# Optimization experiments

Measured on AMD Instinct MI355X. Metric: run time of the kernel, lower is better.

## Reference

```python
import jax, jax.numpy as jnp
import numpy as np

FEATURE_W = 1.0
TRIPLET_W = 1.0
SOFT_W = 1.0
MARGIN = 0.2
TEMP = 1.0
COMMIT_W = 0.1
DISTORT_W = 0.1
STRIDE = 320

B, T, D, K = 8, 1500, 512, 4096


def setup_inputs() -> dict:
    key = jax.random.key(0)
    k1, k2, k3, k4, k5 = jax.random.split(key, 5)
    return {
        "student_features": jax.random.normal(k1, (B, T, D), dtype=jnp.float32),
        "teacher_features": jax.random.normal(k2, (B, T, D), dtype=jnp.float32),
        "teacher_codes": jax.random.randint(k3, (B, T), 0, K),
        "codebook": jax.random.normal(k4, (K, D), dtype=jnp.float32),
        "lengths": jax.random.randint(k5, (B,), 0, T * STRIDE),
    }


def _sq_dists(flat, codebook):
    x2 = jnp.sum(flat * flat, axis=-1, keepdims=True)          # (N,1)
    c2 = jnp.sum(codebook * codebook, axis=-1)[None, :]        # (1,K)
    xc = jnp.einsum("nd,kd->nk", flat, codebook)               # (N,K)
    return jnp.maximum(x2 + c2 - 2.0 * xc, 0.0)


def reference(student_features, teacher_features, teacher_codes, codebook, lengths):
    b, t, d = student_features.shape
    # valid-frame mask from sample lengths
    valid = jnp.minimum(lengths // STRIDE, t)                  # (B,)
    mask = (jnp.arange(t)[None, :] < valid[:, None]).astype(student_features.dtype)  # (B,T)
    msum = jnp.sum(mask)

    # feature loss: masked mean of per-token MSE
    diff = student_features - teacher_features
    feature_loss = jnp.sum(jnp.mean(diff * diff, axis=-1) * mask) / msum

    # triplet loss
    pos_dist = jnp.sqrt(jnp.sum(diff * diff, axis=-1))
    neg_teacher = jnp.roll(teacher_features, shift=1, axis=0)
    nd = student_features - neg_teacher
    neg_dist = jnp.sqrt(jnp.sum(nd * nd, axis=-1))
    triplet = jax.nn.relu(pos_dist - neg_dist + MARGIN)
    triplet_loss = jnp.sum(triplet * mask) / msum

    # soft token (KL distillation over codebook logits)
    s_flat = student_features.reshape(-1, d)                   # (B*T, D)
    t_flat = teacher_features.reshape(-1, d)
    s_logits = -_sq_dists(s_flat, codebook) / TEMP             # (B*T, K)
    t_logits = -_sq_dists(t_flat, codebook) / TEMP
    s_logp = jax.nn.log_softmax(s_logits, axis=-1)
    t_logp = jax.nn.log_softmax(t_logits, axis=-1)
    t_prob = jax.lax.stop_gradient(jnp.exp(t_logp))
    t_logp = jax.lax.stop_gradient(t_logp)
    kl_per_token = jnp.sum(t_prob * (t_logp - s_logp), axis=-1)  # (B*T,)
    flat_mask = mask.reshape(-1)
    soft_loss = jnp.sum(kl_per_token * flat_mask) / msum

    # VQ commitment / distortion (nearest-code quantization)
    codes = jnp.argmax(s_logits, axis=-1)                       # argmin dist == argmax logits
    quantized = codebook[codes].reshape(b, t, d)
    cdiff = student_features - jax.lax.stop_gradient(quantized)
    commitment_loss = jnp.mean(cdiff * cdiff)
    ddiff = jax.lax.stop_gradient(student_features) - quantized
    distortion_loss = jnp.mean(ddiff * ddiff)

    total = (FEATURE_W * feature_loss + TRIPLET_W * triplet_loss
             + SOFT_W * soft_loss + COMMIT_W * commitment_loss
             + DISTORT_W * distortion_loss)
    return total
```

## Files before the change

### kernel.cpp

```cpp
#include <hip/hip_runtime.h>

typedef unsigned short u16;
typedef unsigned int   u32;
typedef float  f32x16 __attribute__((ext_vector_type(16)));
typedef __bf16 bf16x8 __attribute__((ext_vector_type(8)));

#define B_N   8
#define T_N   1500
#define D_N   512
#define K_N   4096
#define NTOK  12000
#define STRD  320

#define X2S_OFF     0u
#define C2_OFF      49152u
#define FEATP_OFF   65536u
#define TRIPP_OFF   67584u
#define STATEP_OFF  71680u
#define SBF_OFF     557056u
#define TBF_OFF     (557056u + 12288000u)
#define CBBF_OFF    (557056u + 24576000u)


__device__ __forceinline__ u16 f2bf(float x){
  u32 u = __float_as_uint(x);
  u32 r = (u + 0x7fffu + ((u >> 16) & 1u)) >> 16;
  return (u16)r;
}

__device__ __forceinline__ void gl_lds16(const void* g, void* l){
  __builtin_amdgcn_global_load_lds(
      (__attribute__((address_space(1))) void*)(g),
      (__attribute__((address_space(3))) void*)(l),
      16, 0, 0);
}

__device__ __forceinline__ void merge_state(float& m, float& Z, float om, float oZ){
  float nm = fmaxf(m, om);
  Z = Z*__expf(m - nm) + oZ*__expf(om - nm);
  m = nm;
}
__device__ __forceinline__ void merge_stateT(float& m, float& Z, float& A,
                                             float om, float oZ, float oA){
  float nm = fmaxf(m, om);
  float e0 = __expf(m - nm), e1 = __expf(om - nm);
  Z = Z*e0 + oZ*e1; A = A*e0 + oA*e1; m = nm;
}

__global__ __launch_bounds__(256) void prep_kernel(
    const float* __restrict__ s, const float* __restrict__ t,
    const float* __restrict__ cb, const int* __restrict__ lengths,
    u16* __restrict__ sbf, u16* __restrict__ tbf, u16* __restrict__ cbbf,
    float* __restrict__ x2s, float* __restrict__ c2,
    float* __restrict__ featP, float* __restrict__ tripP)
{
  const int tid = threadIdx.x;
  const int w = tid >> 6, lane = tid & 63;
  __shared__ float sred[3][32];

  if (blockIdx.x < 375){
    const int tt = blockIdx.x;
    const int t8 = lane >> 3, kpart = lane & 7;
    const int tokL = w*8 + t8;
    const int n = tt*32 + tokL;
    const int b = n / T_N, tok = n - b*T_N;
    const int nr = ((b+7)&7)*T_N + tok;
    const float* srow = s + (size_t)n  * D_N;
    const float* trow = t + (size_t)n  * D_N;
    const float* rrow = t + (size_t)nr * D_N;

    float x2 = 0.f, sd2 = 0.f, nd2 = 0.f;
    uint4 sbq[8], tbq[8];
#pragma unroll
    for (int q = 0; q < 8; ++q){
      const int kl = q*64 + kpart*8;
      float4 a0 = *(const float4*)(srow + kl), a1 = *(const float4*)(srow + kl + 4);
      float4 b0 = *(const float4*)(trow + kl), b1 = *(const float4*)(trow + kl + 4);
      float4 r0 = *(const float4*)(rrow + kl), r1 = *(const float4*)(rrow + kl + 4);
      float sv[8] = {a0.x,a0.y,a0.z,a0.w,a1.x,a1.y,a1.z,a1.w};
      float tv[8] = {b0.x,b0.y,b0.z,b0.w,b1.x,b1.y,b1.z,b1.w};
      float rv[8] = {r0.x,r0.y,r0.z,r0.w,r1.x,r1.y,r1.z,r1.w};
      u16 sb[8], tb[8];
#pragma unroll
      for (int i = 0; i < 8; ++i){
        float d = sv[i] - tv[i]; sd2 += d*d;
        x2 += sv[i]*sv[i];
        float e = sv[i] - rv[i]; nd2 += e*e;
        sb[i] = f2bf(sv[i]); tb[i] = f2bf(tv[i]);
      }
      sbq[q].x = (u32)sb[0] | ((u32)sb[1]<<16); sbq[q].y = (u32)sb[2] | ((u32)sb[3]<<16);
      sbq[q].z = (u32)sb[4] | ((u32)sb[5]<<16); sbq[q].w = (u32)sb[6] | ((u32)sb[7]<<16);
      tbq[q].x = (u32)tb[0] | ((u32)tb[1]<<16); tbq[q].y = (u32)tb[2] | ((u32)tb[3]<<16);
      tbq[q].z = (u32)tb[4] | ((u32)tb[5]<<16); tbq[q].w = (u32)tb[6] | ((u32)tb[7]<<16);
    }
#pragma unroll
    for (int q = 0; q < 8; ++q){
      const int ks = q*4 + (kpart >> 1), kh = kpart & 1;
      const size_t chunk = ((size_t)tt*32 + ks)*64 + kh*32 + tokL;
      ((uint4*)sbf)[chunk] = sbq[q];
      ((uint4*)tbf)[chunk] = tbq[q];
    }
#pragma unroll
    for (int mm = 1; mm < 8; mm <<= 1){
      x2  += __shfl_xor(x2,  mm);
      sd2 += __shfl_xor(sd2, mm);
      nd2 += __shfl_xor(nd2, mm);
    }
    if (kpart == 0){ sred[0][tokL] = x2; sred[1][tokL] = sd2; sred[2][tokL] = nd2; }
    __syncthreads();
    if (tid < 32){
      float X2 = sred[0][tid], SD = sred[1][tid], ND = sred[2][tid];
      int n2 = tt*32 + tid, b2 = n2 / T_N, tk2 = n2 - b2*T_N;
      x2s[n2] = X2;
      int valid = lengths[b2] / STRD; if (valid > T_N) valid = T_N;
      float mf = (tk2 < valid) ? 1.f : 0.f;
      float fp = mf * SD * (1.f/512.f);
      float tp = mf * fmaxf(sqrtf(SD) - sqrtf(ND) + 0.2f, 0.f);
#pragma unroll
      for (int mm = 1; mm < 32; mm <<= 1){ fp += __shfl_xor(fp, mm); tp += __shfl_xor(tp, mm); }
      if (tid == 0){ featP[tt] = fp; tripP[tt] = tp; }
    }
  } else {
    const int idx = blockIdx.x - 375;
    const int ctile = idx*4 + w;
    const int kh = lane >> 5, sp = lane & 31;
    const int ch = ctile >> 6, cg = (ctile >> 3) & 7, ctg = ctile & 7;
    const int code = ctile*32 + sp;
    const float* crow = cb + (size_t)code * D_N;

    float s2 = 0.f;
#pragma unroll
    for (int stp = 0; stp < 32; ++stp){
      const int kc = stp >> 1, ks2 = stp & 1;
      const int k0 = stp*16 + kh*8;
      float4 c0 = *(const float4*)(crow + k0), c1 = *(const float4*)(crow + k0 + 4);
      float cv[8] = {c0.x,c0.y,c0.z,c0.w,c1.x,c1.y,c1.z,c1.w};
      u16 cbv[8];
#pragma unroll
      for (int i = 0; i < 8; ++i){ s2 += cv[i]*cv[i]; cbv[i] = f2bf(cv[i]); }
      uint4 pk;
      pk.x = (u32)cbv[0] | ((u32)cbv[1]<<16); pk.y = (u32)cbv[2] | ((u32)cbv[3]<<16);
      pk.z = (u32)cbv[4] | ((u32)cbv[5]<<16); pk.w = (u32)cbv[6] | ((u32)cbv[7]<<16);
      const size_t off = ((size_t)(ch*128 + cg*16 + kc))*8192 + ctg*1024 + ks2*512 + lane*8;
      *(uint4*)(cbbf + off) = pk;
    }
    s2 += __shfl_xor(s2, 32);
    if (lane < 32) c2[ctile*32 + lane] = s2;
  }
}

__global__ __launch_bounds__(256, 3) void main_kl_kernel(
    const u16* __restrict__ sbf, const u16* __restrict__ tbf,
    const u16* __restrict__ cbbf, const float* __restrict__ c2,
    float* __restrict__ stateP)
{
  __shared__ u16 Bb[2][8192];

  const int tid = threadIdx.x;
  const int w = tid >> 6, lane = tid & 63;
  const int kh = lane >> 5;
  const int tt = blockIdx.x >> 1, ch = blockIdx.x & 1;

  const u16* sA  = sbf  + (size_t)tt*16384;
  const u16* tA  = tbf  + (size_t)tt*16384;
  const u16* cbB = cbbf + (size_t)ch*1048576;

#pragma unroll
  for (int r = 0; r < 4; ++r){
    const int off = (r*256 + tid)*8;
    gl_lds16(cbB + off, &Bb[0][off]);
  }
  bf16x8 fS0 = *(const bf16x8*)(sA + lane*8);
  bf16x8 fS1 = *(const bf16x8*)(sA + 512 + lane*8);
  bf16x8 fT0 = *(const bf16x8*)(tA + lane*8);
  bf16x8 fT1 = *(const bf16x8*)(tA + 512 + lane*8);

  float mS = -3e38f, zS = 0.f, mT = -3e38f, zT = 0.f, aa = 0.f;
  f32x16 aS0, aS1, aT0, aT1;

  for (int c = 0; c < 128; ++c){
    const int kc = c & 15, p = c & 1;
    if (kc == 0){
#pragma unroll
      for (int i = 0; i < 16; ++i){ aS0[i]=0.f; aS1[i]=0.f; aT0[i]=0.f; aT1[i]=0.f; }
    }
    __syncthreads();
    if (c < 127){
      const u16* src = cbB + (size_t)(c+1)*8192;
#pragma unroll
      for (int r = 0; r < 4; ++r){
        const int off = (r*256 + tid)*8;
        gl_lds16(src + off, &Bb[p^1][off]);
      }
    }
    bf16x8 nS0 = fS0, nS1 = fS1, nT0 = fT0, nT1 = fT1;
    if (c < 127){
      const size_t kb = (size_t)((c+1) & 15) * 1024;
      nS0 = *(const bf16x8*)(sA + kb + lane*8);
      nS1 = *(const bf16x8*)(sA + kb + 512 + lane*8);
      nT0 = *(const bf16x8*)(tA + kb + lane*8);
      nT1 = *(const bf16x8*)(tA + kb + 512 + lane*8);
    }

    const u16* bp = &Bb[p][0];
    {
      bf16x8 c0 = *(const bf16x8*)(bp + (w*2+0)*1024 + lane*8);
      bf16x8 c1 = *(const bf16x8*)(bp + (w*2+0)*1024 + 512 + lane*8);
      aS0 = __builtin_amdgcn_mfma_f32_32x32x16_bf16(c0, fS0, aS0, 0, 0, 0);
      aT0 = __builtin_amdgcn_mfma_f32_32x32x16_bf16(c0, fT0, aT0, 0, 0, 0);
      aS0 = __builtin_amdgcn_mfma_f32_32x32x16_bf16(c1, fS1, aS0, 0, 0, 0);
      aT0 = __builtin_amdgcn_mfma_f32_32x32x16_bf16(c1, fT1, aT0, 0, 0, 0);
    }
    {
      bf16x8 c0 = *(const bf16x8*)(bp + (w*2+1)*1024 + lane*8);
      bf16x8 c1 = *(const bf16x8*)(bp + (w*2+1)*1024 + 512 + lane*8);
      aS1 = __builtin_amdgcn_mfma_f32_32x32x16_bf16(c0, fS0, aS1, 0, 0, 0);
      aT1 = __builtin_amdgcn_mfma_f32_32x32x16_bf16(c0, fT0, aT1, 0, 0, 0);
      aS1 = __builtin_amdgcn_mfma_f32_32x32x16_bf16(c1, fS1, aS1, 0, 0, 0);
      aT1 = __builtin_amdgcn_mfma_f32_32x32x16_bf16(c1, fT1, aT1, 0, 0, 0);
    }
    fS0 = nS0; fS1 = nS1; fT0 = nT0; fT1 = nT1;

    if (kc == 15){
      const int cg = c >> 4;
#pragma unroll
      for (int ct = 0; ct < 2; ++ct){
        const f32x16& vS = ct ? aS1 : aS0;
        const f32x16& vT = ct ? aT1 : aT0;
        const int ctg = w*2 + ct;
        const float* c2b = c2 + ch*2048 + cg*256 + ctg*32 + kh*4;
        float4 g0 = *(const float4*)(c2b);
        float4 g1 = *(const float4*)(c2b + 8);
        float4 g2 = *(const float4*)(c2b + 16);
        float4 g3 = *(const float4*)(c2b + 24);
        float c2v[16] = {g0.x,g0.y,g0.z,g0.w, g1.x,g1.y,g1.z,g1.w,
                         g2.x,g2.y,g2.z,g2.w, g3.x,g3.y,g3.z,g3.w};
        float sl[16], tl[16];
#pragma unroll
        for (int i = 0; i < 16; ++i){
          sl[i] = 2.0f*vS[i] - c2v[i];
          tl[i] = 2.0f*vT[i] - c2v[i];
        }
        float ms_t = sl[0], mt_t = tl[0];
#pragma unroll
        for (int i = 1; i < 16; ++i){ ms_t = fmaxf(ms_t, sl[i]); mt_t = fmaxf(mt_t, tl[i]); }
        float nmS = fmaxf(mS, ms_t), nmT = fmaxf(mT, mt_t);
        float esS = __expf(mS - nmS), esT = __expf(mT - nmT);
        zS *= esS; zT *= esT; aa *= esT;
#pragma unroll
        for (int i = 0; i < 16; ++i){
          zS += __expf(sl[i] - nmS);
          float e = __expf(tl[i] - nmT);
          zT += e; aa += e*(tl[i] - sl[i]);
        }
        mS = nmS; mT = nmT;
      }
    }
  }

  {
    float om = __shfl_xor(mS, 32), oZ = __shfl_xor(zS, 32);
    merge_state(mS, zS, om, oZ);
    float omt = __shfl_xor(mT, 32), ozt = __shfl_xor(zT, 32), oA = __shfl_xor(aa, 32);
    merge_stateT(mT, zT, aa, omt, ozt, oA);
  }
  __syncthreads();
  float* wst = (float*)&Bb[0][0];
  if (lane < 32){
    float* pw = wst + (w*32 + lane)*5;
    pw[0] = mS; pw[1] = zS; pw[2] = mT; pw[3] = zT; pw[4] = aa;
  }
  __syncthreads();
  if (tid < 32){
    const float* p0 = wst + tid*5;
    float m_s = p0[0], z_s = p0[1], m_t = p0[2], z_t = p0[3], a = p0[4];
#pragma unroll
    for (int ww = 1; ww < 4; ++ww){
      const float* pw = wst + (ww*32 + tid)*5;
      merge_state(m_s, z_s, pw[0], pw[1]);
      merge_stateT(m_t, z_t, a, pw[2], pw[3], pw[4]);
    }
    const int n = tt*32 + tid;
    stateP[0*24000 + ch*12000 + n] = m_s;
    stateP[1*24000 + ch*12000 + n] = z_s;
    stateP[2*24000 + ch*12000 + n] = m_t;
    stateP[3*24000 + ch*12000 + n] = z_t;
    stateP[4*24000 + ch*12000 + n] = a;
  }
}

__global__ __launch_bounds__(1024) void tail_kernel(
    const float* __restrict__ stateP, const float* __restrict__ x2s,
    const float* __restrict__ featP, const float* __restrict__ tripP,
    const int* __restrict__ lengths, float* __restrict__ out)
{
  const int tid = threadIdx.x;
  double kl_s = 0.0, md_s = 0.0, f = 0.0, tr = 0.0;
  for (int n = tid; n < NTOK; n += 1024){
    float m_s = stateP[0*24000 + n], z_s = stateP[1*24000 + n];
    float m_t = stateP[2*24000 + n], z_t = stateP[3*24000 + n], a = stateP[4*24000 + n];
    merge_state(m_s, z_s, stateP[0*24000 + 12000 + n], stateP[1*24000 + 12000 + n]);
    merge_stateT(m_t, z_t, a, stateP[2*24000 + 12000 + n], stateP[3*24000 + 12000 + n],
                 stateP[4*24000 + 12000 + n]);
    float klv = a / z_t - (m_t + __logf(z_t)) + (m_s + __logf(z_s));
    int b = n / T_N, tk = n - b*T_N;
    int valid = lengths[b] / STRD; if (valid > T_N) valid = T_N;
    if (tk < valid) kl_s += (double)klv;
    md_s += (double)fmaxf(x2s[n] - m_s, 0.f);
  }
  for (int i = tid; i < 375; i += 1024){ f += (double)featP[i]; tr += (double)tripP[i]; }
#pragma unroll
  for (int mm = 1; mm < 64; mm <<= 1){
    kl_s += __shfl_xor(kl_s, mm); md_s += __shfl_xor(md_s, mm);
    f    += __shfl_xor(f,    mm); tr   += __shfl_xor(tr,   mm);
  }
  __shared__ double red[16][4];
  const int w = tid >> 6, lane = tid & 63;
  if (lane == 0){ red[w][0]=kl_s; red[w][1]=md_s; red[w][2]=f; red[w][3]=tr; }
  __syncthreads();
  if (tid == 0){
    double KL=0, MD=0, F=0, TR=0;
    for (int ww = 0; ww < 16; ++ww){ KL+=red[ww][0]; MD+=red[ww][1]; F+=red[ww][2]; TR+=red[ww][3]; }
    long msum = 0;
    for (int b = 0; b < 8; ++b){ int v = lengths[b] / STRD; if (v > T_N) v = T_N; msum += v; }
    double inv = 1.0 / (double)msum;
    double total = F*inv + TR*inv + KL*inv + 0.2 * MD / ((double)B_N * T_N * D_N);
    out[0] = (float)total;
  }
}

extern "C" void kernel_launch(void* const* d_in, const int* in_sizes, int n_in,
                              void* d_out, int out_size, void* d_ws, size_t ws_size,
                              hipStream_t stream)
{
  const float* s  = (const float*)d_in[0];
  const float* t  = (const float*)d_in[1];
  const float* cb = (const float*)d_in[3];
  const int* lengths = (const int*)d_in[4];

  char* ws = (char*)d_ws;
  float* x2s    = (float*)(ws + X2S_OFF);
  float* c2     = (float*)(ws + C2_OFF);
  float* featP  = (float*)(ws + FEATP_OFF);
  float* tripP  = (float*)(ws + TRIPP_OFF);
  float* stateP = (float*)(ws + STATEP_OFF);
  u16* sbf  = (u16*)(ws + SBF_OFF);
  u16* tbf  = (u16*)(ws + TBF_OFF);
  u16* cbbf = (u16*)(ws + CBBF_OFF);

  prep_kernel<<<407, 256, 0, stream>>>(s, t, cb, lengths, sbf, tbf, cbbf,
                                       x2s, c2, featP, tripP);
  main_kl_kernel<<<750, 256, 0, stream>>>(sbf, tbf, cbbf, c2, stateP);
  tail_kernel<<<1, 1024, 0, stream>>>(stateP, x2s, featP, tripP, lengths, (float*)d_out);
}
```

Before: 266.4 us.

## Retile KL GEMM to 64 tokens by 1024 codes per block with LDS-staged activations

Each block of the main kernel now covers 64 tokens (two 32-token tiles) against a quarter of the codebook, instead of 32 tokens against half. Student and teacher bf16 activations are double-buffered in LDS through async global-to-LDS loads rather than read per wave from global memory. Each codebook tile loaded into LDS now feeds twice as many MFMAs, which is meant to cut LDS and global traffic per FLOP. The tail kernel merges four codebook-chunk partial states instead of two. In exchange, accumulator register use doubles, occupancy drops to 2 blocks per SIMD, and the grid is padded to 752 blocks, which makes the last block read past the 12000 tokens and relies on the enlarged workspace offsets.

```diff
diff --git a/kernel.cpp b/kernel.cpp
--- a/kernel.cpp
+++ b/kernel.cpp
@@ -16,10 +16,13 @@
 #define C2_OFF      49152u
 #define FEATP_OFF   65536u
 #define TRIPP_OFF   67584u
-#define STATEP_OFF  71680u
-#define SBF_OFF     557056u
-#define TBF_OFF     (557056u + 12288000u)
-#define CBBF_OFF    (557056u + 24576000u)
+#define STATEP_OFF  69632u
+#define SBF_OFF     1048576u
+#define TBF_OFF     (1048576u + 12320768u)
+#define CBBF_OFF    (1048576u + 24641536u)
+
+#define ST_S1  12032
+#define ST_SQ  48128
 
 
 __device__ __forceinline__ u16 f2bf(float x){
@@ -124,7 +127,7 @@
     const int idx = blockIdx.x - 375;
     const int ctile = idx*4 + w;
     const int kh = lane >> 5, sp = lane & 31;
-    const int ch = ctile >> 6, cg = (ctile >> 3) & 7, ctg = ctile & 7;
+    const int ch = ctile >> 5, cg = (ctile >> 3) & 3, ctg = ctile & 7;
     const int code = ctile*32 + sp;
     const float* crow = cb + (size_t)code * D_N;
 
@@ -141,7 +144,7 @@
       uint4 pk;
       pk.x = (u32)cbv[0] | ((u32)cbv[1]<<16); pk.y = (u32)cbv[2] | ((u32)cbv[3]<<16);
       pk.z = (u32)cbv[4] | ((u32)cbv[5]<<16); pk.w = (u32)cbv[6] | ((u32)cbv[7]<<16);
-      const size_t off = ((size_t)(ch*128 + cg*16 + kc))*8192 + ctg*1024 + ks2*512 + lane*8;
+      const size_t off = ((size_t)(ch*64 + cg*16 + kc))*8192 + ctg*1024 + ks2*512 + lane*8;
       *(uint4*)(cbbf + off) = pk;
     }
     s2 += __shfl_xor(s2, 32);
@@ -149,143 +152,164 @@
   }
 }
 
-__global__ __launch_bounds__(256, 3) void main_kl_kernel(
+__global__ __launch_bounds__(256, 2) void main_kl_kernel(
     const u16* __restrict__ sbf, const u16* __restrict__ tbf,
     const u16* __restrict__ cbbf, const float* __restrict__ c2,
     float* __restrict__ stateP)
 {
+  __shared__ u16 Ab[2][4096];
   __shared__ u16 Bb[2][8192];
 
   const int tid = threadIdx.x;
   const int w = tid >> 6, lane = tid & 63;
-  const int kh = lane >> 5;
-  const int tt = blockIdx.x >> 1, ch = blockIdx.x & 1;
-
-  const u16* sA  = sbf  + (size_t)tt*16384;
-  const u16* tA  = tbf  + (size_t)tt*16384;
-  const u16* cbB = cbbf + (size_t)ch*1048576;
-
-#pragma unroll
-  for (int r = 0; r < 4; ++r){
-    const int off = (r*256 + tid)*8;
-    gl_lds16(cbB + off, &Bb[0][off]);
-  }
-  bf16x8 fS0 = *(const bf16x8*)(sA + lane*8);
-  bf16x8 fS1 = *(const bf16x8*)(sA + 512 + lane*8);
-  bf16x8 fT0 = *(const bf16x8*)(tA + lane*8);
-  bf16x8 fT1 = *(const bf16x8*)(tA + 512 + lane*8);
-
-  float mS = -3e38f, zS = 0.f, mT = -3e38f, zT = 0.f, aa = 0.f;
-  f32x16 aS0, aS1, aT0, aT1;
-
-  for (int c = 0; c < 128; ++c){
-    const int kc = c & 15, p = c & 1;
-    if (kc == 0){
-#pragma unroll
-      for (int i = 0; i < 16; ++i){ aS0[i]=0.f; aS1[i]=0.f; aT0[i]=0.f; aT1[i]=0.f; }
+  const int kh = lane >> 5, sp = lane & 31;
+  const int tt = blockIdx.x >> 2, ch = blockIdx.x & 3;
+
+  const u16* cbB = cbbf + (size_t)ch * 524288;
+  const int piece = (tid >> 7);
+  const int inner = tid & 127;
+
+  {
+#pragma unroll
+    for (int r = 0; r < 4; ++r){
+      const int off = (r*256 + tid)*8;
+      gl_lds16(cbB + off, &Bb[0][off]);
+    }
+#pragma unroll
+    for (int r = 0; r < 2; ++r){
+      const int pc = r*2 + piece;
+      const int tokt = pc >> 1, mat = pc & 1;
+      const u16* base = mat ? tbf : sbf;
+      const size_t srco = ((size_t)(tt*2 + tokt)*32 + 0)*512 + inner*8;
+      gl_lds16(base + srco, &Ab[0][pc*1024 + inner*8]);
+    }
+  }
+
+  float mS[2] = {-3e38f,-3e38f}, zS[2] = {0.f,0.f};
+  float mT[2] = {-3e38f,-3e38f}, zT[2] = {0.f,0.f}, aa[2] = {0.f,0.f};
+  f32x16 a00s, a00t, a01s, a01t, a10s, a10t, a11s, a11t;
+
+  for (int c = 0; c < 64; ++c){
+    const int p = c & 1;
+    if ((c & 15) == 0){
+#pragma unroll
+      for (int i = 0; i < 16; ++i){
+        a00s[i]=0.f; a00t[i]=0.f; a01s[i]=0.f; a01t[i]=0.f;
+        a10s[i]=0.f; a10t[i]=0.f; a11s[i]=0.f; a11t[i]=0.f;
+      }
     }
     __syncthreads();
-    if (c < 127){
-      const u16* src = cbB + (size_t)(c+1)*8192;
+    if (c < 63){
+      const int kc1 = (c+1) & 15;
 #pragma unroll
       for (int r = 0; r < 4; ++r){
         const int off = (r*256 + tid)*8;
-        gl_lds16(src + off, &Bb[p^1][off]);
-      }
-    }
-    bf16x8 nS0 = fS0, nS1 = fS1, nT0 = fT0, nT1 = fT1;
-    if (c < 127){
-      const size_t kb = (size_t)((c+1) & 15) * 1024;
-      nS0 = *(const bf16x8*)(sA + kb + lane*8);
-      nS1 = *(const bf16x8*)(sA + kb + 512 + lane*8);
-      nT0 = *(const bf16x8*)(tA + kb + lane*8);
-      nT1 = *(const bf16x8*)(tA + kb + 512 + lane*8);
-    }
-
+        gl_lds16(cbB + (size_t)(c+1)*8192 + off, &Bb[p^1][off]);
+      }
+#pragma unroll
+      for (int r = 0; r < 2; ++r){
+        const int pc = r*2 + piece;
+        const int tokt = pc >> 1, mat = pc & 1;
+        const u16* base = mat ? tbf : sbf;
+        const size_t srco = ((size_t)(tt*2 + tokt)*32 + kc1*2)*512 + inner*8;
+        gl_lds16(base + srco, &Ab[p^1][pc*1024 + inner*8]);
+      }
+    }
+
+    const u16* ap = &Ab[p][0];
     const u16* bp = &Bb[p][0];
-    {
-      bf16x8 c0 = *(const bf16x8*)(bp + (w*2+0)*1024 + lane*8);
-      bf16x8 c1 = *(const bf16x8*)(bp + (w*2+0)*1024 + 512 + lane*8);
-      aS0 = __builtin_amdgcn_mfma_f32_32x32x16_bf16(c0, fS0, aS0, 0, 0, 0);
-      aT0 = __builtin_amdgcn_mfma_f32_32x32x16_bf16(c0, fT0, aT0, 0, 0, 0);
-      aS0 = __builtin_amdgcn_mfma_f32_32x32x16_bf16(c1, fS1, aS0, 0, 0, 0);
-      aT0 = __builtin_amdgcn_mfma_f32_32x32x16_bf16(c1, fT1, aT0, 0, 0, 0);
-    }
-    {
-      bf16x8 c0 = *(const bf16x8*)(bp + (w*2+1)*1024 + lane*8);
-      bf16x8 c1 = *(const bf16x8*)(bp + (w*2+1)*1024 + 512 + lane*8);
-      aS1 = __builtin_amdgcn_mfma_f32_32x32x16_bf16(c0, fS0, aS1, 0, 0, 0);
-      aT1 = __builtin_amdgcn_mfma_f32_32x32x16_bf16(c0, fT0, aT1, 0, 0, 0);
-      aS1 = __builtin_amdgcn_mfma_f32_32x32x16_bf16(c1, fS1, aS1, 0, 0, 0);
-      aT1 = __builtin_amdgcn_mfma_f32_32x32x16_bf16(c1, fT1, aT1, 0, 0, 0);
-    }
-    fS0 = nS0; fS1 = nS1; fT0 = nT0; fT1 = nT1;
-
-    if (kc == 15){
+#pragma unroll
+    for (int ks = 0; ks < 2; ++ks){
+      bf16x8 b0  = *(const bf16x8*)(bp + (w*2+0)*1024 + ks*512 + lane*8);
+      bf16x8 b1  = *(const bf16x8*)(bp + (w*2+1)*1024 + ks*512 + lane*8);
+      bf16x8 as0 = *(const bf16x8*)(ap + (0*2+0)*1024 + ks*512 + lane*8);
+      bf16x8 at0 = *(const bf16x8*)(ap + (0*2+1)*1024 + ks*512 + lane*8);
+      bf16x8 as1 = *(const bf16x8*)(ap + (1*2+0)*1024 + ks*512 + lane*8);
+      bf16x8 at1 = *(const bf16x8*)(ap + (1*2+1)*1024 + ks*512 + lane*8);
+      a00s = __builtin_amdgcn_mfma_f32_32x32x16_bf16(b0, as0, a00s, 0, 0, 0);
+      a00t = __builtin_amdgcn_mfma_f32_32x32x16_bf16(b0, at0, a00t, 0, 0, 0);
+      a01s = __builtin_amdgcn_mfma_f32_32x32x16_bf16(b0, as1, a01s, 0, 0, 0);
+      a01t = __builtin_amdgcn_mfma_f32_32x32x16_bf16(b0, at1, a01t, 0, 0, 0);
+      a10s = __builtin_amdgcn_mfma_f32_32x32x16_bf16(b1, as0, a10s, 0, 0, 0);
+      a10t = __builtin_amdgcn_mfma_f32_32x32x16_bf16(b1, at0, a10t, 0, 0, 0);
+      a11s = __builtin_amdgcn_mfma_f32_32x32x16_bf16(b1, as1, a11s, 0, 0, 0);
+      a11t = __builtin_amdgcn_mfma_f32_32x32x16_bf16(b1, at1, a11t, 0, 0, 0);
+    }
+
+    if ((c & 15) == 15){
       const int cg = c >> 4;
 #pragma unroll
       for (int ct = 0; ct < 2; ++ct){
-        const f32x16& vS = ct ? aS1 : aS0;
-        const f32x16& vT = ct ? aT1 : aT0;
         const int ctg = w*2 + ct;
-        const float* c2b = c2 + ch*2048 + cg*256 + ctg*32 + kh*4;
+        const float* c2b = c2 + ch*1024 + cg*256 + ctg*32 + kh*4;
         float4 g0 = *(const float4*)(c2b);
         float4 g1 = *(const float4*)(c2b + 8);
         float4 g2 = *(const float4*)(c2b + 16);
         float4 g3 = *(const float4*)(c2b + 24);
         float c2v[16] = {g0.x,g0.y,g0.z,g0.w, g1.x,g1.y,g1.z,g1.w,
                          g2.x,g2.y,g2.z,g2.w, g3.x,g3.y,g3.z,g3.w};
-        float sl[16], tl[16];
-#pragma unroll
-        for (int i = 0; i < 16; ++i){
-          sl[i] = 2.0f*vS[i] - c2v[i];
-          tl[i] = 2.0f*vT[i] - c2v[i];
+#pragma unroll
+        for (int tt_ = 0; tt_ < 2; ++tt_){
+          const f32x16& vS = ct ? (tt_ ? a11s : a10s) : (tt_ ? a01s : a00s);
+          const f32x16& vT = ct ? (tt_ ? a11t : a10t) : (tt_ ? a01t : a00t);
+          float sl[16], tl[16];
+#pragma unroll
+          for (int i = 0; i < 16; ++i){
+            sl[i] = 2.0f*vS[i] - c2v[i];
+            tl[i] = 2.0f*vT[i] - c2v[i];
+          }
+          float ms_t = sl[0], mt_t = tl[0];
+#pragma unroll
+          for (int i = 1; i < 16; ++i){ ms_t = fmaxf(ms_t, sl[i]); mt_t = fmaxf(mt_t, tl[i]); }
+          float nmS = fmaxf(mS[tt_], ms_t), nmT = fmaxf(mT[tt_], mt_t);
+          float esS = __expf(mS[tt_] - nmS), esT = __expf(mT[tt_] - nmT);
+          zS[tt_] *= esS; zT[tt_] *= esT; aa[tt_] *= esT;
+#pragma unroll
+          for (int i = 0; i < 16; ++i){
+            zS[tt_] += __expf(sl[i] - nmS);
+            float e = __expf(tl[i] - nmT);
+            zT[tt_] += e; aa[tt_] += e*(tl[i] - sl[i]);
+          }
+          mS[tt_] = nmS; mT[tt_] = nmT;
         }
-        float ms_t = sl[0], mt_t = tl[0];
-#pragma unroll
-        for (int i = 1; i < 16; ++i){ ms_t = fmaxf(ms_t, sl[i]); mt_t = fmaxf(mt_t, tl[i]); }
-        float nmS = fmaxf(mS, ms_t), nmT = fmaxf(mT, mt_t);
-        float esS = __expf(mS - nmS), esT = __expf(mT - nmT);
-        zS *= esS; zT *= esT; aa *= esT;
-#pragma unroll
-        for (int i = 0; i < 16; ++i){
-          zS += __expf(sl[i] - nmS);
-          float e = __expf(tl[i] - nmT);
-          zT += e; aa += e*(tl[i] - sl[i]);
-        }
-        mS = nmS; mT = nmT;
-      }
-    }
-  }
-
-  {
-    float om = __shfl_xor(mS, 32), oZ = __shfl_xor(zS, 32);
-    merge_state(mS, zS, om, oZ);
-    float omt = __shfl_xor(mT, 32), ozt = __shfl_xor(zT, 32), oA = __shfl_xor(aa, 32);
-    merge_stateT(mT, zT, aa, omt, ozt, oA);
+      }
+    }
+  }
+
+#pragma unroll
+  for (int tt_ = 0; tt_ < 2; ++tt_){
+    float om = __shfl_xor(mS[tt_], 32), oZ = __shfl_xor(zS[tt_], 32);
+    merge_state(mS[tt_], zS[tt_], om, oZ);
+    float omt = __shfl_xor(mT[tt_], 32), ozt = __shfl_xor(zT[tt_], 32),
+          oA  = __shfl_xor(aa[tt_], 32);
+    merge_stateT(mT[tt_], zT[tt_], aa[tt_], omt, ozt, oA);
   }
   __syncthreads();
-  float* wst = (float*)&Bb[0][0];
+  float* wst = (float*)&Ab[0][0];
   if (lane < 32){
-    float* pw = wst + (w*32 + lane)*5;
-    pw[0] = mS; pw[1] = zS; pw[2] = mT; pw[3] = zT; pw[4] = aa;
+#pragma unroll
+    for (int tt_ = 0; tt_ < 2; ++tt_){
+      float* pw = wst + ((w*2 + tt_)*32 + sp)*5;
+      pw[0] = mS[tt_]; pw[1] = zS[tt_]; pw[2] = mT[tt_]; pw[3] = zT[tt_]; pw[4] = aa[tt_];
+    }
   }
   __syncthreads();
-  if (tid < 32){
-    const float* p0 = wst + tid*5;
+  if (tid < 64){
+    const int tokt = tid >> 5, tsp = tid & 31;
+    const float* p0 = wst + ((0*2 + tokt)*32 + tsp)*5;
     float m_s = p0[0], z_s = p0[1], m_t = p0[2], z_t = p0[3], a = p0[4];
 #pragma unroll
     for (int ww = 1; ww < 4; ++ww){
-      const float* pw = wst + (ww*32 + tid)*5;
+      const float* pw = wst + ((ww*2 + tokt)*32 + tsp)*5;
       merge_state(m_s, z_s, pw[0], pw[1]);
       merge_stateT(m_t, z_t, a, pw[2], pw[3], pw[4]);
     }
-    const int n = tt*32 + tid;
-    stateP[0*24000 + ch*12000 + n] = m_s;
-    stateP[1*24000 + ch*12000 + n] = z_s;
-    stateP[2*24000 + ch*12000 + n] = m_t;
-    stateP[3*24000 + ch*12000 + n] = z_t;
-    stateP[4*24000 + ch*12000 + n] = a;
+    const int n = tt*64 + tokt*32 + tsp;
+    stateP[0*ST_SQ + ch*ST_S1 + n] = m_s;
+    stateP[1*ST_SQ + ch*ST_S1 + n] = z_s;
+    stateP[2*ST_SQ + ch*ST_S1 + n] = m_t;
+    stateP[3*ST_SQ + ch*ST_S1 + n] = z_t;
+    stateP[4*ST_SQ + ch*ST_S1 + n] = a;
   }
 }
 
@@ -297,11 +321,14 @@
   const int tid = threadIdx.x;
   double kl_s = 0.0, md_s = 0.0, f = 0.0, tr = 0.0;
   for (int n = tid; n < NTOK; n += 1024){
-    float m_s = stateP[0*24000 + n], z_s = stateP[1*24000 + n];
-    float m_t = stateP[2*24000 + n], z_t = stateP[3*24000 + n], a = stateP[4*24000 + n];
-    merge_state(m_s, z_s, stateP[0*24000 + 12000 + n], stateP[1*24000 + 12000 + n]);
-    merge_stateT(m_t, z_t, a, stateP[2*24000 + 12000 + n], stateP[3*24000 + 12000 + n],
-                 stateP[4*24000 + 12000 + n]);
+    float m_s = stateP[0*ST_SQ + n], z_s = stateP[1*ST_SQ + n];
+    float m_t = stateP[2*ST_SQ + n], z_t = stateP[3*ST_SQ + n], a = stateP[4*ST_SQ + n];
+#pragma unroll
+    for (int chh = 1; chh < 4; ++chh){
+      merge_state(m_s, z_s, stateP[0*ST_SQ + chh*ST_S1 + n], stateP[1*ST_SQ + chh*ST_S1 + n]);
+      merge_stateT(m_t, z_t, a, stateP[2*ST_SQ + chh*ST_S1 + n],
+                   stateP[3*ST_SQ + chh*ST_S1 + n], stateP[4*ST_SQ + chh*ST_S1 + n]);
+    }
     float klv = a / z_t - (m_t + __logf(z_t)) + (m_s + __logf(z_s));
     int b = n / T_N, tk = n - b*T_N;
     int valid = lengths[b] / STRD; if (valid > T_N) valid = T_N;
@@ -350,6 +377,6 @@
 
   prep_kernel<<<407, 256, 0, stream>>>(s, t, cb, lengths, sbf, tbf, cbbf,
                                        x2s, c2, featP, tripP);
-  main_kl_kernel<<<750, 256, 0, stream>>>(sbf, tbf, cbbf, c2, stateP);
+  main_kl_kernel<<<752, 256, 0, stream>>>(sbf, tbf, cbbf, c2, stateP);
   tail_kernel<<<1, 1024, 0, stream>>>(stateP, x2s, featP, tripP, lengths, (float*)d_out);
 }
```

Measured after the change: 442.5 us. +66.1%, slower.

## Split codebook into four chunks, stage tokens in LDS and stream codebook to registers

Applied to the files above, without the earlier changes.

The main KL kernel now splits the codebook four ways instead of two, giving 1500 blocks. Each block stages only the small student/teacher token tiles in LDS (4 KB per buffer instead of 16 KB) and loads its codebook fragments straight from global memory into registers. The tail kernel merges four partial softmax states per token instead of two, and the workspace layout grows to match. This aims at higher occupancy and less LDS traffic, at the cost of more codebook reads from global/L2 per block and twice as many token-tile reloads.

```diff
diff --git a/kernel.cpp b/kernel.cpp
--- a/kernel.cpp
+++ b/kernel.cpp
@@ -16,10 +16,13 @@
 #define C2_OFF      49152u
 #define FEATP_OFF   65536u
 #define TRIPP_OFF   67584u
-#define STATEP_OFF  71680u
-#define SBF_OFF     557056u
-#define TBF_OFF     (557056u + 12288000u)
-#define CBBF_OFF    (557056u + 24576000u)
+#define STATEP_OFF  69632u
+#define SBF_OFF     1048576u
+#define TBF_OFF     (1048576u + 12288000u)
+#define CBBF_OFF    (1048576u + 24576000u)
+
+#define ST_S1  12000
+#define ST_SQ  48000
 
 
 __device__ __forceinline__ u16 f2bf(float x){
@@ -124,7 +127,7 @@
     const int idx = blockIdx.x - 375;
     const int ctile = idx*4 + w;
     const int kh = lane >> 5, sp = lane & 31;
-    const int ch = ctile >> 6, cg = (ctile >> 3) & 7, ctg = ctile & 7;
+    const int ch = ctile >> 5, cg = (ctile >> 3) & 3, ctg = ctile & 7;
     const int code = ctile*32 + sp;
     const float* crow = cb + (size_t)code * D_N;
 
@@ -141,7 +144,7 @@
       uint4 pk;
       pk.x = (u32)cbv[0] | ((u32)cbv[1]<<16); pk.y = (u32)cbv[2] | ((u32)cbv[3]<<16);
       pk.z = (u32)cbv[4] | ((u32)cbv[5]<<16); pk.w = (u32)cbv[6] | ((u32)cbv[7]<<16);
-      const size_t off = ((size_t)(ch*128 + cg*16 + kc))*8192 + ctg*1024 + ks2*512 + lane*8;
+      const size_t off = ((size_t)(ch*64 + cg*16 + kc))*8192 + ctg*1024 + ks2*512 + lane*8;
       *(uint4*)(cbbf + off) = pk;
     }
     s2 += __shfl_xor(s2, 32);
@@ -154,104 +157,98 @@
     const u16* __restrict__ cbbf, const float* __restrict__ c2,
     float* __restrict__ stateP)
 {
-  __shared__ u16 Bb[2][8192];
+  __shared__ u16 Ab[2][2048];
 
   const int tid = threadIdx.x;
   const int w = tid >> 6, lane = tid & 63;
   const int kh = lane >> 5;
-  const int tt = blockIdx.x >> 1, ch = blockIdx.x & 1;
-
-  const u16* sA  = sbf  + (size_t)tt*16384;
-  const u16* tA  = tbf  + (size_t)tt*16384;
-  const u16* cbB = cbbf + (size_t)ch*1048576;
-
-#pragma unroll
-  for (int r = 0; r < 4; ++r){
-    const int off = (r*256 + tid)*8;
-    gl_lds16(cbB + off, &Bb[0][off]);
-  }
-  bf16x8 fS0 = *(const bf16x8*)(sA + lane*8);
-  bf16x8 fS1 = *(const bf16x8*)(sA + 512 + lane*8);
-  bf16x8 fT0 = *(const bf16x8*)(tA + lane*8);
-  bf16x8 fT1 = *(const bf16x8*)(tA + 512 + lane*8);
+  const int blk = blockIdx.x;
+  const int tt = blk % 375, ch = blk / 375;
+
+  const u16* cbB = cbbf + (size_t)ch * 524288;
+  const int mat = tid >> 7, inner = tid & 127;
+  const u16* aSrc = (mat ? tbf : sbf) + (size_t)tt*16384;
+
+  gl_lds16(aSrc + ((size_t)(inner >> 6)*64 + (inner & 63))*8,
+           &Ab[0][mat*1024 + inner*8]);
+  bf16x8 b00, b01, b10, b11;
+  {
+    const u16* rg = cbB;
+    b00 = *(const bf16x8*)(rg + (w*2+0)*1024 +       lane*8);
+    b01 = *(const bf16x8*)(rg + (w*2+0)*1024 + 512 + lane*8);
+    b10 = *(const bf16x8*)(rg + (w*2+1)*1024 +       lane*8);
+    b11 = *(const bf16x8*)(rg + (w*2+1)*1024 + 512 + lane*8);
+  }
 
   float mS = -3e38f, zS = 0.f, mT = -3e38f, zT = 0.f, aa = 0.f;
-  f32x16 aS0, aS1, aT0, aT1;
-
-  for (int c = 0; c < 128; ++c){
+  f32x16 a0s, a0t, a1s, a1t;
+
+  for (int c = 0; c < 64; ++c){
     const int kc = c & 15, p = c & 1;
     if (kc == 0){
 #pragma unroll
-      for (int i = 0; i < 16; ++i){ aS0[i]=0.f; aS1[i]=0.f; aT0[i]=0.f; aT1[i]=0.f; }
+      for (int i = 0; i < 16; ++i){ a0s[i]=0.f; a0t[i]=0.f; a1s[i]=0.f; a1t[i]=0.f; }
     }
     __syncthreads();
-    if (c < 127){
-      const u16* src = cbB + (size_t)(c+1)*8192;
-#pragma unroll
-      for (int r = 0; r < 4; ++r){
-        const int off = (r*256 + tid)*8;
-        gl_lds16(src + off, &Bb[p^1][off]);
-      }
-    }
-    bf16x8 nS0 = fS0, nS1 = fS1, nT0 = fT0, nT1 = fT1;
-    if (c < 127){
-      const size_t kb = (size_t)((c+1) & 15) * 1024;
-      nS0 = *(const bf16x8*)(sA + kb + lane*8);
-      nS1 = *(const bf16x8*)(sA + kb + 512 + lane*8);
-      nT0 = *(const bf16x8*)(tA + kb + lane*8);
-      nT1 = *(const bf16x8*)(tA + kb + 512 + lane*8);
-    }
-
-    const u16* bp = &Bb[p][0];
-    {
-      bf16x8 c0 = *(const bf16x8*)(bp + (w*2+0)*1024 + lane*8);
-      bf16x8 c1 = *(const bf16x8*)(bp + (w*2+0)*1024 + 512 + lane*8);
-      aS0 = __builtin_amdgcn_mfma_f32_32x32x16_bf16(c0, fS0, aS0, 0, 0, 0);
-      aT0 = __builtin_amdgcn_mfma_f32_32x32x16_bf16(c0, fT0, aT0, 0, 0, 0);
-      aS0 = __builtin_amdgcn_mfma_f32_32x32x16_bf16(c1, fS1, aS0, 0, 0, 0);
-      aT0 = __builtin_amdgcn_mfma_f32_32x32x16_bf16(c1, fT1, aT0, 0, 0, 0);
-    }
-    {
-      bf16x8 c0 = *(const bf16x8*)(bp + (w*2+1)*1024 + lane*8);
-      bf16x8 c1 = *(const bf16x8*)(bp + (w*2+1)*1024 + 512 + lane*8);
-      aS1 = __builtin_amdgcn_mfma_f32_32x32x16_bf16(c0, fS0, aS1, 0, 0, 0);
-      aT1 = __builtin_amdgcn_mfma_f32_32x32x16_bf16(c0, fT0, aT1, 0, 0, 0);
-      aS1 = __builtin_amdgcn_mfma_f32_32x32x16_bf16(c1, fS1, aS1, 0, 0, 0);
-      aT1 = __builtin_amdgcn_mfma_f32_32x32x16_bf16(c1, fT1, aT1, 0, 0, 0);
-    }
-    fS0 = nS0; fS1 = nS1; fT0 = nT0; fT1 = nT1;
+    if (c < 63){
+      const int kc1 = (c+1) & 15;
+      gl_lds16(aSrc + (((size_t)kc1*2 + (inner >> 6))*64 + (inner & 63))*8,
+               &Ab[p^1][mat*1024 + inner*8]);
+    }
+    bf16x8 n00 = b00, n01 = b01, n10 = b10, n11 = b11;
+    if (c < 63){
+      const u16* rg = cbB + (size_t)(c+1)*8192;
+      n00 = *(const bf16x8*)(rg + (w*2+0)*1024 +       lane*8);
+      n01 = *(const bf16x8*)(rg + (w*2+0)*1024 + 512 + lane*8);
+      n10 = *(const bf16x8*)(rg + (w*2+1)*1024 +       lane*8);
+      n11 = *(const bf16x8*)(rg + (w*2+1)*1024 + 512 + lane*8);
+    }
+
+    const u16* ap = &Ab[p][0];
+    bf16x8 as0 = *(const bf16x8*)(ap +        lane*8);
+    bf16x8 at0 = *(const bf16x8*)(ap + 1024 + lane*8);
+    bf16x8 as1 = *(const bf16x8*)(ap +  512 + lane*8);
+    bf16x8 at1 = *(const bf16x8*)(ap + 1536 + lane*8);
+    a0s = __builtin_amdgcn_mfma_f32_32x32x16_bf16(b00, as0, a0s, 0, 0, 0);
+    a0t = __builtin_amdgcn_mfma_f32_32x32x16_bf16(b00, at0, a0t, 0, 0, 0);
+    a1s = __builtin_amdgcn_mfma_f32_32x32x16_bf16(b10, as0, a1s, 0, 0, 0);
+    a1t = __builtin_amdgcn_mfma_f32_32x32x16_bf16(b10, at0, a1t, 0, 0, 0);
+    a0s = __builtin_amdgcn_mfma_f32_32x32x16_bf16(b01, as1, a0s, 0, 0, 0);
+    a0t = __builtin_amdgcn_mfma_f32_32x32x16_bf16(b01, at1, a0t, 0, 0, 0);
+    a1s = __builtin_amdgcn_mfma_f32_32x32x16_bf16(b11, as1, a1s, 0, 0, 0);
+    a1t = __builtin_amdgcn_mfma_f32_32x32x16_bf16(b11, at1, a1t, 0, 0, 0);
+    b00 = n00; b01 = n01; b10 = n10; b11 = n11;
 
     if (kc == 15){
       const int cg = c >> 4;
 #pragma unroll
       for (int ct = 0; ct < 2; ++ct){
-        const f32x16& vS = ct ? aS1 : aS0;
-        const f32x16& vT = ct ? aT1 : aT0;
+        const f32x16& vS = ct ? a1s : a0s;
+        const f32x16& vT = ct ? a1t : a0t;
         const int ctg = w*2 + ct;
-        const float* c2b = c2 + ch*2048 + cg*256 + ctg*32 + kh*4;
+        const float* c2b = c2 + ch*1024 + cg*256 + ctg*32 + kh*4;
         float4 g0 = *(const float4*)(c2b);
         float4 g1 = *(const float4*)(c2b + 8);
         float4 g2 = *(const float4*)(c2b + 16);
         float4 g3 = *(const float4*)(c2b + 24);
         float c2v[16] = {g0.x,g0.y,g0.z,g0.w, g1.x,g1.y,g1.z,g1.w,
                          g2.x,g2.y,g2.z,g2.w, g3.x,g3.y,g3.z,g3.w};
-        float sl[16], tl[16];
+        float ms_t = -3e38f, mt_t = -3e38f;
 #pragma unroll
         for (int i = 0; i < 16; ++i){
-          sl[i] = 2.0f*vS[i] - c2v[i];
-          tl[i] = 2.0f*vT[i] - c2v[i];
+          ms_t = fmaxf(ms_t, 2.0f*vS[i] - c2v[i]);
+          mt_t = fmaxf(mt_t, 2.0f*vT[i] - c2v[i]);
         }
-        float ms_t = sl[0], mt_t = tl[0];
-#pragma unroll
-        for (int i = 1; i < 16; ++i){ ms_t = fmaxf(ms_t, sl[i]); mt_t = fmaxf(mt_t, tl[i]); }
         float nmS = fmaxf(mS, ms_t), nmT = fmaxf(mT, mt_t);
         float esS = __expf(mS - nmS), esT = __expf(mT - nmT);
         zS *= esS; zT *= esT; aa *= esT;
 #pragma unroll
         for (int i = 0; i < 16; ++i){
-          zS += __expf(sl[i] - nmS);
-          float e = __expf(tl[i] - nmT);
-          zT += e; aa += e*(tl[i] - sl[i]);
+          float sl = 2.0f*vS[i] - c2v[i];
+          float tl = 2.0f*vT[i] - c2v[i];
+          zS += __expf(sl - nmS);
+          float e = __expf(tl - nmT);
+          zT += e; aa += e*(tl - sl);
         }
         mS = nmS; mT = nmT;
       }
@@ -265,7 +262,7 @@
     merge_stateT(mT, zT, aa, omt, ozt, oA);
   }
   __syncthreads();
-  float* wst = (float*)&Bb[0][0];
+  float* wst = (float*)&Ab[0][0];
   if (lane < 32){
     float* pw = wst + (w*32 + lane)*5;
     pw[0] = mS; pw[1] = zS; pw[2] = mT; pw[3] = zT; pw[4] = aa;
@@ -281,11 +278,11 @@
       merge_stateT(m_t, z_t, a, pw[2], pw[3], pw[4]);
     }
     const int n = tt*32 + tid;
-    stateP[0*24000 + ch*12000 + n] = m_s;
-    stateP[1*24000 + ch*12000 + n] = z_s;
-    stateP[2*24000 + ch*12000 + n] = m_t;
-    stateP[3*24000 + ch*12000 + n] = z_t;
-    stateP[4*24000 + ch*12000 + n] = a;
+    stateP[0*ST_SQ + ch*ST_S1 + n] = m_s;
+    stateP[1*ST_SQ + ch*ST_S1 + n] = z_s;
+    stateP[2*ST_SQ + ch*ST_S1 + n] = m_t;
+    stateP[3*ST_SQ + ch*ST_S1 + n] = z_t;
+    stateP[4*ST_SQ + ch*ST_S1 + n] = a;
   }
 }
 
@@ -297,11 +294,14 @@
   const int tid = threadIdx.x;
   double kl_s = 0.0, md_s = 0.0, f = 0.0, tr = 0.0;
   for (int n = tid; n < NTOK; n += 1024){
-    float m_s = stateP[0*24000 + n], z_s = stateP[1*24000 + n];
-    float m_t = stateP[2*24000 + n], z_t = stateP[3*24000 + n], a = stateP[4*24000 + n];
-    merge_state(m_s, z_s, stateP[0*24000 + 12000 + n], stateP[1*24000 + 12000 + n]);
-    merge_stateT(m_t, z_t, a, stateP[2*24000 + 12000 + n], stateP[3*24000 + 12000 + n],
-                 stateP[4*24000 + 12000 + n]);
+    float m_s = stateP[0*ST_SQ + n], z_s = stateP[1*ST_SQ + n];
+    float m_t = stateP[2*ST_SQ + n], z_t = stateP[3*ST_SQ + n], a = stateP[4*ST_SQ + n];
+#pragma unroll
+    for (int chh = 1; chh < 4; ++chh){
+      merge_state(m_s, z_s, stateP[0*ST_SQ + chh*ST_S1 + n], stateP[1*ST_SQ + chh*ST_S1 + n]);
+      merge_stateT(m_t, z_t, a, stateP[2*ST_SQ + chh*ST_S1 + n],
+                   stateP[3*ST_SQ + chh*ST_S1 + n], stateP[4*ST_SQ + chh*ST_S1 + n]);
+    }
     float klv = a / z_t - (m_t + __logf(z_t)) + (m_s + __logf(z_s));
     int b = n / T_N, tk = n - b*T_N;
     int valid = lengths[b] / STRD; if (valid > T_N) valid = T_N;
@@ -350,6 +350,6 @@
 
   prep_kernel<<<407, 256, 0, stream>>>(s, t, cb, lengths, sbf, tbf, cbbf,
                                        x2s, c2, featP, tripP);
-  main_kl_kernel<<<750, 256, 0, stream>>>(sbf, tbf, cbbf, c2, stateP);
+  main_kl_kernel<<<1500, 256, 0, stream>>>(sbf, tbf, cbbf, c2, stateP);
   tail_kernel<<<1, 1024, 0, stream>>>(stateP, x2s, featP, tripP, lengths, (float*)d_out);
 }
```

Result: faster. 246.8 us (-7.3%).
